# Kernel optimization log

Hardware: AMD Instinct MI355X
Metric: run time of the kernel (lower is better)

Reference implementation:

```python
import jax, jax.numpy as jnp
import numpy as np

B, C, H, W = 32, 192, 32, 32
CH, STRIDE = 8, 2
FEAT = CH * (H // STRIDE) * (W // STRIDE)  # 8*16*16 = 2048


def setup_inputs() -> dict:
    key = jax.random.key(0)
    ks = jax.random.split(key, 7)
    inp = jax.random.normal(ks[0], (B, C, H, W), jnp.float32)
    w_left_out = jax.random.normal(ks[1], (B, C, H, W), jnp.float32)
    conv_w = jax.random.normal(ks[2], (CH, C, 3, 3), jnp.float32) * 0.05
    conv_b = jnp.zeros((CH,), jnp.float32)
    # small scale keeps diag(U) moderate so exp(s) stays finite
    lin_w = jax.random.normal(ks[3], (C * C, FEAT), jnp.float32) * 0.01
    lin_b = jax.random.normal(ks[4], (C * C,), jnp.float32) * 0.1
    s_sign = jnp.sign(jax.random.normal(ks[5], (C,), jnp.float32))
    return dict(inp=inp, w_left_out=w_left_out, conv_w=conv_w, conv_b=conv_b,
                lin_w=lin_w, lin_b=lin_b, s_sign=s_sign)


def _cond_net(x, conv_w, conv_b, lin_w, lin_b):
    # Conv2d(C->CH, k=3, stride=2, pad=1) + ReLU + Flatten + Linear(FEAT -> C*C)
    h = jax.lax.conv_general_dilated(
        x, conv_w, window_strides=(STRIDE, STRIDE), padding=((1, 1), (1, 1)),
        dimension_numbers=('NCHW', 'OIHW', 'NCHW'))
    h = jax.nn.relu(h + conv_b[None, :, None, None])
    return h.reshape(x.shape[0], -1) @ lin_w.T + lin_b  # [B, C*C]


def reference(inp, w_left_out, conv_w, conv_b, lin_w, lin_b, s_sign):
    b, c, height, width = inp.shape
    cond = _cond_net(w_left_out, conv_w, conv_b, lin_w, lin_b)
    mats = cond.reshape(b, c, c)
    # batched LU: a = p @ l @ u (scipy convention, unit-diag l)
    p, l, u = jax.vmap(jax.scipy.linalg.lu)(mats)
    s = jnp.diagonal(u, axis1=1, axis2=2)          # [B, C] raw diag(U)
    eye = jnp.eye(c, dtype=inp.dtype)
    l_full = jnp.tril(l, -1) + eye                  # l * l_mask + I
    u_full = jnp.triu(u, 1) + (s_sign[None, :] * jnp.exp(s))[..., None] * eye
    weight = p @ l_full @ u_full                    # [B, C, C]
    # batched 1x1 conv == per-sample GEMM over spatial positions
    out = jnp.einsum('bij,bjhw->bihw', weight, inp)
    log_w = jnp.mean(jnp.sum(s, axis=1))            # sum(w_s) averaged over batch
    log_det = (height * width) * log_w
    return out, log_det
```

## Files before the change

### kernel.cpp

```cpp
#include <hip/hip_runtime.h>
#include <math.h>


#define NFEAT 2048
#define NN    36864

__global__ __launch_bounds__(256) void conv_kernel(const float* __restrict__ w,
                                                   const float* __restrict__ cw,
                                                   float* __restrict__ hpart) {
  int blk = blockIdx.x;
  int ph = blk & 1;
  int bc = blk >> 1;
  int b = bc >> 2, cs = bc & 3;
  int tid = threadIdx.x;
  int pix = tid & 127;
  int chh = tid >> 7;
  int oy = (ph << 3) + (pix >> 4);
  int ox = pix & 15;
  __shared__ float wlds[8 * 48 * 9];
  for (int idx = tid; idx < 8 * 48 * 9; idx += 256) {
    int ch = idx / 432, rem = idx - ch * 432;
    int c = rem / 9, kk = rem - c * 9;
    wlds[idx] = cw[ch * 1728 + (cs * 48 + c) * 9 + kk];
  }
  __syncthreads();
  float acc[4];
#pragma unroll
  for (int j = 0; j < 4; ++j) acc[j] = 0.f;
  const float* img0 = w + (((size_t)b * 192 + cs * 48) << 10);
  for (int c = 0; c < 48; ++c) {
    const float* img = img0 + ((size_t)c << 10);
    float iv[9];
#pragma unroll
    for (int ky = 0; ky < 3; ++ky)
#pragma unroll
      for (int kx = 0; kx < 3; ++kx) {
        int iy = 2 * oy - 1 + ky, ix = 2 * ox - 1 + kx;
        bool ok = (iy >= 0) & (iy < 32) & (ix >= 0) & (ix < 32);
        iv[ky * 3 + kx] = ok ? img[iy * 32 + ix] : 0.f;
      }
#pragma unroll
    for (int j = 0; j < 4; ++j) {
      int ch = (chh << 2) + j;
      const float* wp = &wlds[(ch * 48 + c) * 9];
      float s = acc[j];
#pragma unroll
      for (int t = 0; t < 9; ++t) s = fmaf(iv[t], wp[t], s);
      acc[j] = s;
    }
  }
  size_t base = ((size_t)(cs * 32 + b) << 11) + (oy << 4) + ox;
#pragma unroll
  for (int j = 0; j < 4; ++j) hpart[base + ((size_t)((chh << 2) + j) << 8)] = acc[j];
}

__global__ __launch_bounds__(256) void hreduce_kernel(const float* __restrict__ hpart,
                                                      const float* __restrict__ cb,
                                                      float* __restrict__ h_bt) {
  int g = blockIdx.x * 256 + threadIdx.x;
  int k = g & 2047, b = g >> 11;
  float s = 0.f;
#pragma unroll
  for (int cs = 0; cs < 4; ++cs) s += hpart[(((size_t)(cs * 32 + b)) << 11) + k];
  s += cb[k >> 8];
  s = fmaxf(s, 0.f);
  h_bt[g] = s;
}

#define WROW(r) ((r) * 68 + (((r) >> 3) << 2))
__global__ __launch_bounds__(128) void linear_kernel(const float* __restrict__ h_bt,
                                                     const float* __restrict__ lw,
                                                     float* __restrict__ qpart) {
  __shared__ float Wbuf[8768];
  __shared__ float Hbuf[2192];
  int tid = threadIdx.x;
  int blk = blockIdx.x;
  int q = blk & 3;
  int tile = blk >> 2;
  int n0 = tile << 7;
  int kqb = q << 9;
  int bp = tid & 7;
  int ng = tid >> 3;
  int nb = ng << 3;
  int bb0 = bp << 2;
  float acc[32];
#pragma unroll
  for (int i = 0; i < 32; ++i) acc[i] = 0.f;

  for (int kc = 0; kc < 8; ++kc) {
    int koff = kqb + (kc << 6);
#pragma unroll
    for (int j = 0; j < 16; ++j) {
      int f = tid + (j << 7);
      int row = f >> 4, c4 = (f & 15) << 2;
      *(float4*)(Wbuf + WROW(row) + c4) =
          *(const float4*)(lw + (size_t)(n0 + row) * 2048 + koff + c4);
    }
#pragma unroll
    for (int j = 0; j < 4; ++j) {
      int f = tid + (j << 7);
      int bi = f >> 4, c4 = (f & 15) << 2;
      *(float4*)(Hbuf + WROW(bi) + c4) =
          *(const float4*)(h_bt + (size_t)bi * 2048 + koff + c4);
    }
    __syncthreads();
#pragma unroll 2
    for (int k4 = 0; k4 < 16; ++k4) {
      int kk = k4 << 2;
      float4 h0 = *(const float4*)(Hbuf + WROW(bb0 + 0) + kk);
      float4 h1 = *(const float4*)(Hbuf + WROW(bb0 + 1) + kk);
      float4 h2 = *(const float4*)(Hbuf + WROW(bb0 + 2) + kk);
      float4 h3 = *(const float4*)(Hbuf + WROW(bb0 + 3) + kk);
#pragma unroll
      for (int j = 0; j < 8; ++j) {
        float4 w4 = *(const float4*)(Wbuf + WROW(nb + j) + kk);
        float s0 = acc[j * 4 + 0], s1 = acc[j * 4 + 1];
        float s2 = acc[j * 4 + 2], s3 = acc[j * 4 + 3];
        s0 = fmaf(w4.x, h0.x, s0); s0 = fmaf(w4.y, h0.y, s0);
        s0 = fmaf(w4.z, h0.z, s0); s0 = fmaf(w4.w, h0.w, s0);
        s1 = fmaf(w4.x, h1.x, s1); s1 = fmaf(w4.y, h1.y, s1);
        s1 = fmaf(w4.z, h1.z, s1); s1 = fmaf(w4.w, h1.w, s1);
        s2 = fmaf(w4.x, h2.x, s2); s2 = fmaf(w4.y, h2.y, s2);
        s2 = fmaf(w4.z, h2.z, s2); s2 = fmaf(w4.w, h2.w, s2);
        s3 = fmaf(w4.x, h3.x, s3); s3 = fmaf(w4.y, h3.y, s3);
        s3 = fmaf(w4.z, h3.z, s3); s3 = fmaf(w4.w, h3.w, s3);
        acc[j * 4 + 0] = s0; acc[j * 4 + 1] = s1;
        acc[j * 4 + 2] = s2; acc[j * 4 + 3] = s3;
      }
    }
    __syncthreads();
  }
#pragma unroll
  for (int i = 0; i < 4; ++i) {
    float* p = qpart + (size_t)q * 1179648 + (size_t)(bb0 + i) * NN + n0 + nb;
    *(float4*)(p + 0) = make_float4(acc[0 * 4 + i], acc[1 * 4 + i], acc[2 * 4 + i], acc[3 * 4 + i]);
    *(float4*)(p + 4) = make_float4(acc[4 * 4 + i], acc[5 * 4 + i], acc[6 * 4 + i], acc[7 * 4 + i]);
  }
}

__global__ __launch_bounds__(256) void combine_kernel(const float* __restrict__ qpart,
                                                      const float* __restrict__ lb,
                                                      float* __restrict__ mats) {
  int blk = blockIdx.x;
  int b = blk / 18, nt = blk - b * 18;
  int n = (nt << 11) + (threadIdx.x << 3);
  size_t base = (size_t)b * NN + n;
#pragma unroll
  for (int h = 0; h < 2; ++h) {
    float4 q0 = *(const float4*)(qpart + 0 * 1179648 + base + 4 * h);
    float4 q1 = *(const float4*)(qpart + 1 * 1179648 + base + 4 * h);
    float4 q2 = *(const float4*)(qpart + 2 * 1179648 + base + 4 * h);
    float4 q3 = *(const float4*)(qpart + 3 * 1179648 + base + 4 * h);
    float4 bb = *(const float4*)(lb + n + 4 * h);
    float4 o;
    o.x = ((q0.x + q1.x) + q2.x) + q3.x + bb.x;
    o.y = ((q0.y + q1.y) + q2.y) + q3.y + bb.y;
    o.z = ((q0.z + q1.z) + q2.z) + q3.z + bb.z;
    o.w = ((q0.w + q1.w) + q2.w) + q3.w + bb.w;
    *(float4*)(mats + base + 4 * h) = o;
  }
}

#define CAT_(A, B) A##B
#define CAT(A, B) CAT_(A, B)
#define PR_0(R) CAT(pA, R).x
#define PR_1(R) CAT(pA, R).y
#define PR_2(R) CAT(pA, R).z
#define PR_3(R) CAT(pA, R).w
#define PR_4(R) CAT(pB, R).x
#define PR_5(R) CAT(pB, R).y
#define PR_6(R) CAT(pB, R).z
#define PR_7(R) CAT(pB, R).w
#define PR(R, K) CAT(PR_, K)(R)
#define UU_0 uA.x
#define UU_1 uA.y
#define UU_2 uA.z
#define UU_3 uA.w
#define UU_4 uB.x
#define UU_5 uB.y
#define UU_6 uB.z
#define UU_7 uB.w
#define UU(K) CAT(UU_, K)
#define UPDJ(R, J) PR(R, J) = fmaf(-m, UU(J), PR(R, J));
#define TAIL_0(R) UPDJ(R,1) UPDJ(R,2) UPDJ(R,3) UPDJ(R,4) UPDJ(R,5) UPDJ(R,6) UPDJ(R,7)
#define TAIL_1(R) UPDJ(R,2) UPDJ(R,3) UPDJ(R,4) UPDJ(R,5) UPDJ(R,6) UPDJ(R,7)
#define TAIL_2(R) UPDJ(R,3) UPDJ(R,4) UPDJ(R,5) UPDJ(R,6) UPDJ(R,7)
#define TAIL_3(R) UPDJ(R,4) UPDJ(R,5) UPDJ(R,6) UPDJ(R,7)
#define TAIL_4(R) UPDJ(R,5) UPDJ(R,6) UPDJ(R,7)
#define TAIL_5(R) UPDJ(R,6) UPDJ(R,7)
#define TAIL_6(R) UPDJ(R,7)
#define TAIL_7(R)
#define UPDROW(R, KK, kg)                                                      \
  if (CAT(lg, R) > (kg)) {                                                     \
    float m = PR(R, KK) * recip;                                               \
    PR(R, KK) = m;                                                             \
    CAT(TAIL_, KK)(R)                                                          \
  }
#define PSTEP(KK) {                                                            \
  const int kg = kpP + KK;                                                     \
  float bv = -1.f; int br = 0x7fffffff;                                        \
  { float v = fabsf(PR(0,KK)); if (lg0 >= kg && (v > bv || (v == bv && lg0 < br))) { bv = v; br = lg0; } } \
  { float v = fabsf(PR(1,KK)); if (lg1 >= kg && (v > bv || (v == bv && lg1 < br))) { bv = v; br = lg1; } } \
  { float v = fabsf(PR(2,KK)); if (lg2 >= kg && (v > bv || (v == bv && lg2 < br))) { bv = v; br = lg2; } } \
  for (int msk = 1; msk <= 32; msk <<= 1) {                                    \
    float ov = __shfl_xor(bv, msk, 64);                                        \
    int obr = __shfl_xor(br, msk, 64);                                         \
    if (ov > bv || (ov == bv && obr < br)) { bv = ov; br = obr; }              \
  }                                                                            \
  bool own0 = (lg0 == br), own1 = (lg1 == br), own2 = (lg2 == br);             \
  float4 sA = own1 ? pA1 : (own2 ? pA2 : pA0);                                 \
  float4 sB = own1 ? pB1 : (own2 ? pB2 : pB0);                                 \
  int owner = (int)__ffsll(__ballot(own0 | own1 | own2)) - 1;                  \
  float4 uA, uB;                                                               \
  uA.x = __shfl(sA.x, owner); uA.y = __shfl(sA.y, owner);                      \
  uA.z = __shfl(sA.z, owner); uA.w = __shfl(sA.w, owner);                      \
  uB.x = __shfl(sB.x, owner); uB.y = __shfl(sB.y, owner);                      \
  uB.z = __shfl(sB.z, owner); uB.w = __shfl(sB.w, owner);                      \
  float piv = UU(KK);                                                          \
  float recip = 1.0f / piv;                                                    \
  if (tid == 0) {                                                              \
    diagU[kg] = piv;                                                           \
    int t0 = rowmap[kg], t1 = rowmap[br];                                      \
    rowmap[kg] = t1; rowmap[br] = t0;                                          \
  }                                                                            \
  lg0 = (lg0 == kg) ? br : ((lg0 == br) ? kg : lg0);                           \
  lg1 = (lg1 == kg) ? br : ((lg1 == br) ? kg : lg1);                           \
  lg2 = (lg2 == kg) ? br : ((lg2 == br) ? kg : lg2);                           \
  UPDROW(0, KK, kg)                                                            \
  UPDROW(1, KK, kg)                                                            \
  UPDROW(2, KK, kg)                                                            \
}
#define FMA4(D, M, S) {                                                        \
  float mm = (M);                                                              \
  D.x = fmaf(-mm, S.x, D.x); D.y = fmaf(-mm, S.y, D.y);                        \
  D.z = fmaf(-mm, S.z, D.z); D.w = fmaf(-mm, S.w, D.w);                        \
}
#define PANEL(KPV) {                                                           \
  const int kpP = (KPV);                                                       \
  const int pcP = kpP >> 2;                                                    \
  float4 pA0 = As4[tid * 49 + pcP],         pB0 = As4[tid * 49 + pcP + 1];     \
  float4 pA1 = As4[(tid + 64) * 49 + pcP],  pB1 = As4[(tid + 64) * 49 + pcP + 1]; \
  float4 pA2 = As4[(tid + 128) * 49 + pcP], pB2 = As4[(tid + 128) * 49 + pcP + 1]; \
  PSTEP(0) PSTEP(1) PSTEP(2) PSTEP(3) PSTEP(4) PSTEP(5) PSTEP(6) PSTEP(7)     \
  As4[tid * 49 + pcP] = pA0;         As4[tid * 49 + pcP + 1] = pB0;            \
  As4[(tid + 64) * 49 + pcP] = pA1;  As4[(tid + 64) * 49 + pcP + 1] = pB1;     \
  As4[(tid + 128) * 49 + pcP] = pA2; As4[(tid + 128) * 49 + pcP + 1] = pB2;    \
}
#define TRSM8REG(U0, U1, U2, U3, U4, U5, U6, U7, COLQ)                         \
  float4 u40 = As4[U0 * 49 + (COLQ)], u41 = As4[U1 * 49 + (COLQ)];             \
  float4 u42 = As4[U2 * 49 + (COLQ)], u43 = As4[U3 * 49 + (COLQ)];             \
  float4 u44 = As4[U4 * 49 + (COLQ)], u45 = As4[U5 * 49 + (COLQ)];             \
  float4 u46 = As4[U6 * 49 + (COLQ)], u47 = As4[U7 * 49 + (COLQ)];             \
  { float4 la = As4[U1 * 49 + pc];                                             \
    FMA4(u41, la.x, u40) }                                                     \
  { float4 la = As4[U2 * 49 + pc];                                             \
    FMA4(u42, la.x, u40) FMA4(u42, la.y, u41) }                                \
  { float4 la = As4[U3 * 49 + pc];                                             \
    FMA4(u43, la.x, u40) FMA4(u43, la.y, u41) FMA4(u43, la.z, u42) }           \
  { float4 la = As4[U4 * 49 + pc];                                             \
    FMA4(u44, la.x, u40) FMA4(u44, la.y, u41) FMA4(u44, la.z, u42) FMA4(u44, la.w, u43) } \
  { float4 la = As4[U5 * 49 + pc]; float4 lb2 = As4[U5 * 49 + pc + 1];         \
    FMA4(u45, la.x, u40) FMA4(u45, la.y, u41) FMA4(u45, la.z, u42) FMA4(u45, la.w, u43) \
    FMA4(u45, lb2.x, u44) }                                                    \
  { float4 la = As4[U6 * 49 + pc]; float4 lb2 = As4[U6 * 49 + pc + 1];         \
    FMA4(u46, la.x, u40) FMA4(u46, la.y, u41) FMA4(u46, la.z, u42) FMA4(u46, la.w, u43) \
    FMA4(u46, lb2.x, u44) FMA4(u46, lb2.y, u45) }                              \
  { float4 la = As4[U7 * 49 + pc]; float4 lb2 = As4[U7 * 49 + pc + 1];         \
    FMA4(u47, la.x, u40) FMA4(u47, la.y, u41) FMA4(u47, la.z, u42) FMA4(u47, la.w, u43) \
    FMA4(u47, lb2.x, u44) FMA4(u47, lb2.y, u45) FMA4(u47, lb2.z, u46) }

__global__ __launch_bounds__(768, 1) void lu_kernel(float* __restrict__ A0,
                                                    const float* __restrict__ ssign,
                                                    float* __restrict__ ssum) {
  __shared__ float4 As4[192 * 49];
  __shared__ int rowmap[192];
  __shared__ float diagU[192];
  __shared__ float4 dval4[48];
  float* dvalf = (float*)dval4;
  int b = blockIdx.x;
  int tid = threadIdx.x;
  float* __restrict__ A = A0 + (size_t)b * NN;

#pragma unroll
  for (int j = 0; j < 12; ++j) {
    int chunk = tid + 768 * j;
    int row = chunk / 48, q = chunk - row * 48;
    As4[row * 49 + q] = *(const float4*)(A + row * 192 + 4 * q);
  }
  for (int i = tid; i < 192; i += 768) rowmap[i] = i;
  __syncthreads();

  int lg0 = tid, lg1 = tid + 64, lg2 = tid + 128;

  if (tid < 64) { PANEL(0) }
  __syncthreads();

  const int slot = tid & 15;

  for (int p = 0; p < 23; ++p) {
    const int kp = p << 3;
    const int pc = kp >> 2;
    const int qp1 = pc + 2;

    {
      const int col = qp1 + (tid >= 384 ? 1 : 0);
      const int rsl = tid - (tid >= 384 ? 384 : 0);
      const int s = kp + 8 + rsl;
      if (s < 192) {
        const int ua0 = rowmap[kp + 0], ua1 = rowmap[kp + 1];
        const int ua2 = rowmap[kp + 2], ua3 = rowmap[kp + 3];
        const int ua4 = rowmap[kp + 4], ua5 = rowmap[kp + 5];
        const int ua6 = rowmap[kp + 6], ua7 = rowmap[kp + 7];
        TRSM8REG(ua0, ua1, ua2, ua3, ua4, ua5, ua6, ua7, col)
        int phys = rowmap[s];
        float4 la = As4[phys * 49 + pc];
        float4 lb2 = As4[phys * 49 + pc + 1];
        float4 c = As4[phys * 49 + col];
        FMA4(c, la.x, u40) FMA4(c, la.y, u41) FMA4(c, la.z, u42) FMA4(c, la.w, u43)
        FMA4(c, lb2.x, u44) FMA4(c, lb2.y, u45) FMA4(c, lb2.z, u46) FMA4(c, lb2.w, u47)
        As4[phys * 49 + col] = c;
      }
    }
    int php0, php1, php2, php3, php4, php5, php6, php7, php8, php9, php10, php11;
#define SNAP(I) CAT(php, I) = rowmap[slot + (I << 4)];
    SNAP(0) SNAP(1) SNAP(2) SNAP(3) SNAP(4) SNAP(5) SNAP(6)
    SNAP(7) SNAP(8) SNAP(9) SNAP(10) SNAP(11)
#undef SNAP
    __syncthreads();

    if (tid < 64) {
      PANEL(kp + 8)
    } else {
      const int ncols = 44 - pc;
      if (ncols > 0) {
        const int g = (tid >> 4) - 4;
        const int nparts = 44 / ncols;
        const int part = g / ncols;
        const int colIdx = g - part * ncols;
        if (part < nparts) {
          const int q = pc + 4 + colIdx;
          const int ub0 = rowmap[kp + 0], ub1 = rowmap[kp + 1];
          const int ub2 = rowmap[kp + 2], ub3 = rowmap[kp + 3];
          const int ub4 = rowmap[kp + 4], ub5 = rowmap[kp + 5];
          const int ub6 = rowmap[kp + 6], ub7 = rowmap[kp + 7];
          TRSM8REG(ub0, ub1, ub2, ub3, ub4, ub5, ub6, ub7, q)
#define GEMMROW(I) {                                                           \
          int s = slot + (I << 4);                                             \
          if ((I % nparts) == part && s >= kp + 8) {                           \
            int phys = CAT(php, I);                                            \
            float4 la = As4[phys * 49 + pc];                                   \
            float4 lb2 = As4[phys * 49 + pc + 1];                              \
            float4 c = As4[phys * 49 + q];                                     \
            FMA4(c, la.x, u40) FMA4(c, la.y, u41) FMA4(c, la.z, u42) FMA4(c, la.w, u43) \
            FMA4(c, lb2.x, u44) FMA4(c, lb2.y, u45) FMA4(c, lb2.z, u46) FMA4(c, lb2.w, u47) \
            As4[phys * 49 + q] = c;                                            \
          }                                                                    \
        }
          GEMMROW(0) GEMMROW(1) GEMMROW(2) GEMMROW(3) GEMMROW(4) GEMMROW(5)
          GEMMROW(6) GEMMROW(7) GEMMROW(8) GEMMROW(9) GEMMROW(10) GEMMROW(11)
#undef GEMMROW
        }
      }
    }
    __syncthreads();
  }

  if (tid == 0) {
    float s = 0.f;
    for (int i = 0; i < 192; ++i) s += diagU[i];
    ssum[b] = s;
  }
  if (tid < 192) dvalf[tid] = ssign[tid] * expf(diagU[tid]) - diagU[tid];
  __syncthreads();
  {
    const int r = tid >> 2;
    const int tq = tid & 3;
    int i = r;
    int phys = rowmap[r];
    float di = dvalf[i];
    float* __restrict__ G = A + (size_t)phys * 192;
    int qi = i >> 2;
    for (int j = 0; j < 12; ++j) {
      int q = tq + 4 * j;
      if (q > qi) continue;
      float4 g4 = *(float4*)(G + 4 * q);
      float4 a4 = As4[phys * 49 + q];
      float4 d4 = dval4[q];
      if (q == qi) {
        int c0 = 4 * q;
        g4.x = (c0 + 0 < i) ? g4.x + a4.x * d4.x : ((c0 + 0 == i) ? g4.x + di : g4.x);
        g4.y = (c0 + 1 < i) ? g4.y + a4.y * d4.y : ((c0 + 1 == i) ? g4.y + di : g4.y);
        g4.z = (c0 + 2 < i) ? g4.z + a4.z * d4.z : ((c0 + 2 == i) ? g4.z + di : g4.z);
        g4.w = (c0 + 3 < i) ? g4.w + a4.w * d4.w : ((c0 + 3 == i) ? g4.w + di : g4.w);
      } else {
        g4.x += a4.x * d4.x;
        g4.y += a4.y * d4.y;
        g4.z += a4.z * d4.z;
        g4.w += a4.w * d4.w;
      }
      *(float4*)(G + 4 * q) = g4;
    }
  }
}

__global__ __launch_bounds__(256) void out_kernel(const float* __restrict__ wt,
                                                  const float* __restrict__ inp,
                                                  const float* __restrict__ ssum,
                                                  float* __restrict__ out) {
  int blk = blockIdx.x;
  int b = blk / 24, rem = blk % 24;
  int it = rem >> 3, jt = rem & 7;
  int i0 = it << 6, hw0 = jt << 7;
  int tid = threadIdx.x;
  int tx = tid & 31, ty = tid >> 5;
  __shared__ float wldsT[32 * 68];
  __shared__ float xlds[32 * 128];
  const float* wb = wt + (size_t)b * NN;
  const float* xb = inp + (((size_t)b * 192) << 10);
  float acc[8][4];
#pragma unroll
  for (int r = 0; r < 8; ++r)
#pragma unroll
    for (int c = 0; c < 4; ++c) acc[r][c] = 0.f;
  for (int kc = 0; kc < 6; ++kc) {
    __syncthreads();
#pragma unroll
    for (int j = 0; j < 2; ++j) {
      int f4 = tid + (j << 8);
      int row = f4 >> 3, c4 = (f4 & 7) << 2;
      float4 v = *(const float4*)(wb + (size_t)(i0 + row) * 192 + (kc << 5) + c4);
      wldsT[(c4 + 0) * 68 + row] = v.x;
      wldsT[(c4 + 1) * 68 + row] = v.y;
      wldsT[(c4 + 2) * 68 + row] = v.z;
      wldsT[(c4 + 3) * 68 + row] = v.w;
    }
#pragma unroll
    for (int j = 0; j < 4; ++j) {
      int f4 = tid + (j << 8);
      int row = f4 >> 5, c4 = (f4 & 31) << 2;
      float4 v = *(const float4*)(xb + (((size_t)(kc << 5) + row) << 10) + hw0 + c4);
      *(float4*)(xlds + (row << 7) + c4) = v;
    }
    __syncthreads();
#pragma unroll 4
    for (int k = 0; k < 32; ++k) {
      float4 xv = *(const float4*)(xlds + (k << 7) + (tx << 2));
      float4 wa = *(const float4*)(wldsT + k * 68 + ty * 8);
      float4 wbv = *(const float4*)(wldsT + k * 68 + ty * 8 + 4);
      acc[0][0] = fmaf(wa.x, xv.x, acc[0][0]);
      acc[0][1] = fmaf(wa.x, xv.y, acc[0][1]);
      acc[0][2] = fmaf(wa.x, xv.z, acc[0][2]);
      acc[0][3] = fmaf(wa.x, xv.w, acc[0][3]);
      acc[1][0] = fmaf(wa.y, xv.x, acc[1][0]);
      acc[1][1] = fmaf(wa.y, xv.y, acc[1][1]);
      acc[1][2] = fmaf(wa.y, xv.z, acc[1][2]);
      acc[1][3] = fmaf(wa.y, xv.w, acc[1][3]);
      acc[2][0] = fmaf(wa.z, xv.x, acc[2][0]);
      acc[2][1] = fmaf(wa.z, xv.y, acc[2][1]);
      acc[2][2] = fmaf(wa.z, xv.z, acc[2][2]);
      acc[2][3] = fmaf(wa.z, xv.w, acc[2][3]);
      acc[3][0] = fmaf(wa.w, xv.x, acc[3][0]);
      acc[3][1] = fmaf(wa.w, xv.y, acc[3][1]);
      acc[3][2] = fmaf(wa.w, xv.z, acc[3][2]);
      acc[3][3] = fmaf(wa.w, xv.w, acc[3][3]);
      acc[4][0] = fmaf(wbv.x, xv.x, acc[4][0]);
      acc[4][1] = fmaf(wbv.x, xv.y, acc[4][1]);
      acc[4][2] = fmaf(wbv.x, xv.z, acc[4][2]);
      acc[4][3] = fmaf(wbv.x, xv.w, acc[4][3]);
      acc[5][0] = fmaf(wbv.y, xv.x, acc[5][0]);
      acc[5][1] = fmaf(wbv.y, xv.y, acc[5][1]);
      acc[5][2] = fmaf(wbv.y, xv.z, acc[5][2]);
      acc[5][3] = fmaf(wbv.y, xv.w, acc[5][3]);
      acc[6][0] = fmaf(wbv.z, xv.x, acc[6][0]);
      acc[6][1] = fmaf(wbv.z, xv.y, acc[6][1]);
      acc[6][2] = fmaf(wbv.z, xv.z, acc[6][2]);
      acc[6][3] = fmaf(wbv.z, xv.w, acc[6][3]);
      acc[7][0] = fmaf(wbv.w, xv.x, acc[7][0]);
      acc[7][1] = fmaf(wbv.w, xv.y, acc[7][1]);
      acc[7][2] = fmaf(wbv.w, xv.z, acc[7][2]);
      acc[7][3] = fmaf(wbv.w, xv.w, acc[7][3]);
    }
  }
  float* ob = out + (((size_t)b * 192 + i0 + ty * 8) << 10) + hw0 + (tx << 2);
#pragma unroll
  for (int r = 0; r < 8; ++r) {
    float4 v = make_float4(acc[r][0], acc[r][1], acc[r][2], acc[r][3]);
    *(float4*)(ob + ((size_t)r << 10)) = v;
  }
  if (blk == 0 && tid == 0) {
    float s = 0.f;
    for (int i = 0; i < 32; ++i) s += ssum[i];
    out[6291456] = 32.f * s;
  }
}

extern "C" void kernel_launch(void* const* d_in, const int* in_sizes, int n_in,
                              void* d_out, int out_size, void* d_ws, size_t ws_size,
                              hipStream_t stream) {
  const float* inp = (const float*)d_in[0];
  const float* wlo = (const float*)d_in[1];
  const float* cw  = (const float*)d_in[2];
  const float* cb  = (const float*)d_in[3];
  const float* lw  = (const float*)d_in[4];
  const float* lb  = (const float*)d_in[5];
  const float* ss  = (const float*)d_in[6];
  float* out = (float*)d_out;
  float* ws = (float*)d_ws;
  float* hpart = ws;
  float* h_bt  = ws + 262144;
  float* mats  = ws + 327680;
  float* ssum  = ws + 1507328;
  float* qpart = out;
  hipLaunchKernelGGL(conv_kernel,    dim3(256),  dim3(256), 0, stream, wlo, cw, hpart);
  hipLaunchKernelGGL(hreduce_kernel, dim3(256),  dim3(256), 0, stream, hpart, cb, h_bt);
  hipLaunchKernelGGL(linear_kernel,  dim3(1152), dim3(128), 0, stream, h_bt, lw, qpart);
  hipLaunchKernelGGL(combine_kernel, dim3(576),  dim3(256), 0, stream, qpart, lb, mats);
  hipLaunchKernelGGL(lu_kernel,      dim3(32),   dim3(768), 0, stream, mats, ss, ssum);
  hipLaunchKernelGGL(out_kernel,     dim3(768),  dim3(256), 0, stream, mats, inp, ssum, out);
}
```

Baseline: 394.9 us.

## Fuse hreduce into linear load and combine into LU kernel

Removes the hreduce and combine kernels. The conv partial sums are now reduced, biased and ReLU'd while the linear kernel loads its H tile, and the four split-K linear partials plus bias are summed directly inside the LU kernel. This saves two launches and one intermediate round trip for h and for mats. In exchange, each linear block recomputes the h reduction, and the LU kernel (only 32 blocks) reads the four partial buffers twice, once for the load and once for the final write-back, which may leave those global reads poorly parallelised.

```diff
diff --git a/kernel.cpp b/kernel.cpp
--- a/kernel.cpp
+++ b/kernel.cpp
@@ -54,21 +54,9 @@
   for (int j = 0; j < 4; ++j) hpart[base + ((size_t)((chh << 2) + j) << 8)] = acc[j];
 }
 
-__global__ __launch_bounds__(256) void hreduce_kernel(const float* __restrict__ hpart,
-                                                      const float* __restrict__ cb,
-                                                      float* __restrict__ h_bt) {
-  int g = blockIdx.x * 256 + threadIdx.x;
-  int k = g & 2047, b = g >> 11;
-  float s = 0.f;
-#pragma unroll
-  for (int cs = 0; cs < 4; ++cs) s += hpart[(((size_t)(cs * 32 + b)) << 11) + k];
-  s += cb[k >> 8];
-  s = fmaxf(s, 0.f);
-  h_bt[g] = s;
-}
-
 #define WROW(r) ((r) * 68 + (((r) >> 3) << 2))
-__global__ __launch_bounds__(128) void linear_kernel(const float* __restrict__ h_bt,
+__global__ __launch_bounds__(128) void linear_kernel(const float* __restrict__ hpart,
+                                                     const float* __restrict__ cb,
                                                      const float* __restrict__ lw,
                                                      float* __restrict__ qpart) {
   __shared__ float Wbuf[8768];
@@ -100,8 +88,18 @@
     for (int j = 0; j < 4; ++j) {
       int f = tid + (j << 7);
       int bi = f >> 4, c4 = (f & 15) << 2;
-      *(float4*)(Hbuf + WROW(bi) + c4) =
-          *(const float4*)(h_bt + (size_t)bi * 2048 + koff + c4);
+      int kk2 = koff + c4;
+      float4 p0 = *(const float4*)(hpart + (((size_t)(0 * 32 + bi)) << 11) + kk2);
+      float4 p1 = *(const float4*)(hpart + (((size_t)(1 * 32 + bi)) << 11) + kk2);
+      float4 p2 = *(const float4*)(hpart + (((size_t)(2 * 32 + bi)) << 11) + kk2);
+      float4 p3 = *(const float4*)(hpart + (((size_t)(3 * 32 + bi)) << 11) + kk2);
+      float cbv = cb[kk2 >> 8];
+      float4 s;
+      s.x = 0.f; s.x += p0.x; s.x += p1.x; s.x += p2.x; s.x += p3.x; s.x += cbv; s.x = fmaxf(s.x, 0.f);
+      s.y = 0.f; s.y += p0.y; s.y += p1.y; s.y += p2.y; s.y += p3.y; s.y += cbv; s.y = fmaxf(s.y, 0.f);
+      s.z = 0.f; s.z += p0.z; s.z += p1.z; s.z += p2.z; s.z += p3.z; s.z += cbv; s.z = fmaxf(s.z, 0.f);
+      s.w = 0.f; s.w += p0.w; s.w += p1.w; s.w += p2.w; s.w += p3.w; s.w += cbv; s.w = fmaxf(s.w, 0.f);
+      *(float4*)(Hbuf + WROW(bi) + c4) = s;
     }
     __syncthreads();
 #pragma unroll 2
@@ -135,29 +133,6 @@
     float* p = qpart + (size_t)q * 1179648 + (size_t)(bb0 + i) * NN + n0 + nb;
     *(float4*)(p + 0) = make_float4(acc[0 * 4 + i], acc[1 * 4 + i], acc[2 * 4 + i], acc[3 * 4 + i]);
     *(float4*)(p + 4) = make_float4(acc[4 * 4 + i], acc[5 * 4 + i], acc[6 * 4 + i], acc[7 * 4 + i]);
-  }
-}
-
-__global__ __launch_bounds__(256) void combine_kernel(const float* __restrict__ qpart,
-                                                      const float* __restrict__ lb,
-                                                      float* __restrict__ mats) {
-  int blk = blockIdx.x;
-  int b = blk / 18, nt = blk - b * 18;
-  int n = (nt << 11) + (threadIdx.x << 3);
-  size_t base = (size_t)b * NN + n;
-#pragma unroll
-  for (int h = 0; h < 2; ++h) {
-    float4 q0 = *(const float4*)(qpart + 0 * 1179648 + base + 4 * h);
-    float4 q1 = *(const float4*)(qpart + 1 * 1179648 + base + 4 * h);
-    float4 q2 = *(const float4*)(qpart + 2 * 1179648 + base + 4 * h);
-    float4 q3 = *(const float4*)(qpart + 3 * 1179648 + base + 4 * h);
-    float4 bb = *(const float4*)(lb + n + 4 * h);
-    float4 o;
-    o.x = ((q0.x + q1.x) + q2.x) + q3.x + bb.x;
-    o.y = ((q0.y + q1.y) + q2.y) + q3.y + bb.y;
-    o.z = ((q0.z + q1.z) + q2.z) + q3.z + bb.z;
-    o.w = ((q0.w + q1.w) + q2.w) + q3.w + bb.w;
-    *(float4*)(mats + base + 4 * h) = o;
   }
 }
 
@@ -269,9 +244,11 @@
     FMA4(u47, la.x, u40) FMA4(u47, la.y, u41) FMA4(u47, la.z, u42) FMA4(u47, la.w, u43) \
     FMA4(u47, lb2.x, u44) FMA4(u47, lb2.y, u45) FMA4(u47, lb2.z, u46) }
 
-__global__ __launch_bounds__(768, 1) void lu_kernel(float* __restrict__ A0,
+__global__ __launch_bounds__(768, 1) void lu_kernel(const float* __restrict__ qpart,
+                                                    const float* __restrict__ lbp,
                                                     const float* __restrict__ ssign,
-                                                    float* __restrict__ ssum) {
+                                                    float* __restrict__ ssum,
+                                                    float* __restrict__ mats) {
   __shared__ float4 As4[192 * 49];
   __shared__ int rowmap[192];
   __shared__ float diagU[192];
@@ -279,13 +256,25 @@
   float* dvalf = (float*)dval4;
   int b = blockIdx.x;
   int tid = threadIdx.x;
-  float* __restrict__ A = A0 + (size_t)b * NN;
+  float* __restrict__ A = mats + (size_t)b * NN;
+  const size_t qb = (size_t)b * NN;
 
 #pragma unroll
   for (int j = 0; j < 12; ++j) {
     int chunk = tid + 768 * j;
     int row = chunk / 48, q = chunk - row * 48;
-    As4[row * 49 + q] = *(const float4*)(A + row * 192 + 4 * q);
+    size_t n = (size_t)row * 192 + 4 * q;
+    float4 q0 = *(const float4*)(qpart + 0 * 1179648 + qb + n);
+    float4 q1 = *(const float4*)(qpart + 1 * 1179648 + qb + n);
+    float4 q2 = *(const float4*)(qpart + 2 * 1179648 + qb + n);
+    float4 q3 = *(const float4*)(qpart + 3 * 1179648 + qb + n);
+    float4 bb2 = *(const float4*)(lbp + n);
+    float4 m;
+    m.x = ((q0.x + q1.x) + q2.x) + q3.x + bb2.x;
+    m.y = ((q0.y + q1.y) + q2.y) + q3.y + bb2.y;
+    m.z = ((q0.z + q1.z) + q2.z) + q3.z + bb2.z;
+    m.w = ((q0.w + q1.w) + q2.w) + q3.w + bb2.w;
+    As4[row * 49 + q] = m;
   }
   for (int i = tid; i < 192; i += 768) rowmap[i] = i;
   __syncthreads();
@@ -383,7 +372,17 @@
     for (int j = 0; j < 12; ++j) {
       int q = tq + 4 * j;
       if (q > qi) continue;
-      float4 g4 = *(float4*)(G + 4 * q);
+      size_t n = (size_t)phys * 192 + 4 * q;
+      float4 e0 = *(const float4*)(qpart + 0 * 1179648 + qb + n);
+      float4 e1 = *(const float4*)(qpart + 1 * 1179648 + qb + n);
+      float4 e2 = *(const float4*)(qpart + 2 * 1179648 + qb + n);
+      float4 e3 = *(const float4*)(qpart + 3 * 1179648 + qb + n);
+      float4 bb2 = *(const float4*)(lbp + n);
+      float4 g4;
+      g4.x = ((e0.x + e1.x) + e2.x) + e3.x + bb2.x;
+      g4.y = ((e0.y + e1.y) + e2.y) + e3.y + bb2.y;
+      g4.z = ((e0.z + e1.z) + e2.z) + e3.z + bb2.z;
+      g4.w = ((e0.w + e1.w) + e2.w) + e3.w + bb2.w;
       float4 a4 = As4[phys * 49 + q];
       float4 d4 = dval4[q];
       if (q == qi) {
@@ -398,6 +397,22 @@
         g4.z += a4.z * d4.z;
         g4.w += a4.w * d4.w;
       }
+      *(float4*)(G + 4 * q) = g4;
+    }
+    for (int j = 0; j < 12; ++j) {
+      int q = tq + 4 * j;
+      if (q <= qi) continue;
+      size_t n = (size_t)phys * 192 + 4 * q;
+      float4 e0 = *(const float4*)(qpart + 0 * 1179648 + qb + n);
+      float4 e1 = *(const float4*)(qpart + 1 * 1179648 + qb + n);
+      float4 e2 = *(const float4*)(qpart + 2 * 1179648 + qb + n);
+      float4 e3 = *(const float4*)(qpart + 3 * 1179648 + qb + n);
+      float4 bb2 = *(const float4*)(lbp + n);
+      float4 g4;
+      g4.x = ((e0.x + e1.x) + e2.x) + e3.x + bb2.x;
+      g4.y = ((e0.y + e1.y) + e2.y) + e3.y + bb2.y;
+      g4.z = ((e0.z + e1.z) + e2.z) + e3.z + bb2.z;
+      g4.w = ((e0.w + e1.w) + e2.w) + e3.w + bb2.w;
       *(float4*)(G + 4 * q) = g4;
     }
   }
@@ -507,14 +522,11 @@
   float* out = (float*)d_out;
   float* ws = (float*)d_ws;
   float* hpart = ws;
-  float* h_bt  = ws + 262144;
   float* mats  = ws + 327680;
   float* ssum  = ws + 1507328;
   float* qpart = out;
-  hipLaunchKernelGGL(conv_kernel,    dim3(256),  dim3(256), 0, stream, wlo, cw, hpart);
-  hipLaunchKernelGGL(hreduce_kernel, dim3(256),  dim3(256), 0, stream, hpart, cb, h_bt);
-  hipLaunchKernelGGL(linear_kernel,  dim3(1152), dim3(128), 0, stream, h_bt, lw, qpart);
-  hipLaunchKernelGGL(combine_kernel, dim3(576),  dim3(256), 0, stream, qpart, lb, mats);
-  hipLaunchKernelGGL(lu_kernel,      dim3(32),   dim3(768), 0, stream, mats, ss, ssum);
-  hipLaunchKernelGGL(out_kernel,     dim3(768),  dim3(256), 0, stream, mats, inp, ssum, out);
-}
+  hipLaunchKernelGGL(conv_kernel,   dim3(256),  dim3(256), 0, stream, wlo, cw, hpart);
+  hipLaunchKernelGGL(linear_kernel, dim3(1152), dim3(128), 0, stream, hpart, cb, lw, qpart);
+  hipLaunchKernelGGL(lu_kernel,     dim3(32),   dim3(768), 0, stream, qpart, lb, ss, ssum, mats);
+  hipLaunchKernelGGL(out_kernel,    dim3(768),  dim3(256), 0, stream, mats, inp, ssum, out);
+}
```

Result: slower. 425.4 us (+7.7%).
